# Kernel tuning notes

Measured on AMD Instinct MI355X. Metric: run time of the kernel, lower is better.

The kernel has to match this reference:

```python
import jax, jax.numpy as jnp
import numpy as np


def setup_inputs() -> dict:
    key = jax.random.key(0)
    k1, k2 = jax.random.split(key)
    N, D_IN, D_OUT, R = 500000, 128, 128, 8
    inputs = jax.random.normal(k1, (N, D_IN), dtype=jnp.float32)
    # glorot-uniform-ish init for relation weights
    limit = np.sqrt(6.0 / (D_IN + D_OUT)).astype(np.float32)
    relation_weights = jax.random.uniform(k2, (R, D_IN, D_OUT), dtype=jnp.float32, minval=-limit, maxval=limit)
    relation_scales = jnp.ones((R, 1), dtype=jnp.float32)
    return {"inputs": inputs, "relation_weights": relation_weights, "relation_scales": relation_scales}


def reference(inputs, relation_weights, relation_scales):
    # Original: sum_i  inputs @ (W_i * s_i)
    # Algebraically identical: inputs @ sum_i (W_i * s_i) -> one GEMM.
    # scales: [R,1] -> broadcast over [R, d_in, d_out]
    W_eff = jnp.sum(relation_weights * relation_scales[:, :, None], axis=0)  # [d_in, d_out]
    return inputs @ W_eff  # [N, d_out]
```

## Files before the change

### kernel.cpp

```cpp
#include <hip/hip_runtime.h>

typedef __attribute__((ext_vector_type(8))) short short8;
typedef __attribute__((ext_vector_type(4))) float f32x4;

__device__ __forceinline__ short f2bf(float f) {
    unsigned u = __builtin_bit_cast(unsigned, f);
    u += 0x7fffu + ((u >> 16) & 1u);
    return (short)(u >> 16);
}

__global__ void weff_kernel(const float* __restrict__ W,
                            const float* __restrict__ S,
                            short* __restrict__ WT) {
    int idx = blockIdx.x * 256 + threadIdx.x;
    int k = idx >> 7;
    int n = idx & 127;
    float acc = 0.f;
#pragma unroll
    for (int r = 0; r < 8; ++r) acc += S[r] * W[r * 16384 + idx];
    WT[n * 128 + k] = f2bf(acc);
}

#define BSTRIDE 136

__global__ __launch_bounds__(256, 4) void gemm_kernel(const float* __restrict__ A,
                                                      const short* __restrict__ WT,
                                                      float* __restrict__ C,
                                                      int N) {
    __shared__ __align__(16) short Bs[128 * BSTRIDE];

    int tid = threadIdx.x;
#pragma unroll
    for (int it = 0; it < 8; ++it) {
        int chunk = it * 256 + tid;
        int n  = chunk >> 4;
        int kc = chunk & 15;
        *(short8*)&Bs[n * BSTRIDE + kc * 8] = ((const short8*)WT)[chunk];
    }
    __syncthreads();

    int wave = tid >> 6;
    int lane = tid & 63;
    int quad = lane >> 4;
    int r16  = lane & 15;

    long m0   = (long)blockIdx.x * 64 + wave * 16;
    long rowA = m0 + r16;
    long rowAc = rowA < N ? rowA : (long)(N - 1);
    const float* arow = A + rowAc * 128;

    f32x4 acc[8];
#pragma unroll
    for (int t = 0; t < 8; ++t) acc[t] = (f32x4)(0.f);

#pragma unroll
    for (int kk = 0; kk < 4; ++kk) {
        int k = kk * 32 + quad * 8;
        float4 p = *(const float4*)(arow + k);
        float4 q = *(const float4*)(arow + k + 4);
        short8 afrag;
        afrag[0] = f2bf(p.x); afrag[1] = f2bf(p.y);
        afrag[2] = f2bf(p.z); afrag[3] = f2bf(p.w);
        afrag[4] = f2bf(q.x); afrag[5] = f2bf(q.y);
        afrag[6] = f2bf(q.z); afrag[7] = f2bf(q.w);
#pragma unroll
        for (int t = 0; t < 8; ++t) {
            short8 bfrag = *(const short8*)&Bs[(t * 16 + r16) * BSTRIDE + k];
            acc[t] = __builtin_amdgcn_mfma_f32_16x16x32_bf16(afrag, bfrag, acc[t], 0, 0, 0);
        }
    }

#pragma unroll
    for (int reg = 0; reg < 4; ++reg) {
        long row = m0 + quad * 4 + reg;
        if (row < N) {
            float* crow = C + row * 128;
#pragma unroll
            for (int t = 0; t < 8; ++t) crow[t * 16 + r16] = acc[t][reg];
        }
    }
}

extern "C" void kernel_launch(void* const* d_in, const int* in_sizes, int n_in,
                              void* d_out, int out_size, void* d_ws, size_t ws_size,
                              hipStream_t stream) {
    const float* inputs = (const float*)d_in[0];
    const float* W      = (const float*)d_in[1];
    const float* S      = (const float*)d_in[2];
    float* out = (float*)d_out;
    short* WT  = (short*)d_ws;

    int N = in_sizes[0] / 128;

    weff_kernel<<<64, 256, 0, stream>>>(W, S, WT);
    int grid = (N + 63) / 64;
    gemm_kernel<<<grid, 256, 0, stream>>>(inputs, WT, out, N);
}
```

Baseline: 416.2 us.

## Double rows per wave and stage output through LDS for vectorized stores

Each wave now computes two 16-row M fragments, so every B fragment read from LDS feeds two MFMAs and each block covers 128 rows, which halves the number of blocks and the per-block B staging. The epilogue writes accumulators into padded LDS and then emits coalesced 16-byte global stores per row, replacing scattered 4-byte stores. The cost is more accumulator registers (64 floats per thread), which could reduce occupancy under the launch bounds, plus an extra barrier and an LDS round trip in the epilogue.

```diff
diff --git a/kernel.cpp b/kernel.cpp
--- a/kernel.cpp
+++ b/kernel.cpp
@@ -22,12 +22,15 @@
 }
 
 #define BSTRIDE 136
+#define CSTRIDE 132
+#define SMEM_BYTES 34816
 
 __global__ __launch_bounds__(256, 4) void gemm_kernel(const float* __restrict__ A,
                                                       const short* __restrict__ WT,
                                                       float* __restrict__ C,
                                                       int N) {
-    __shared__ __align__(16) short Bs[128 * BSTRIDE];
+    __shared__ __align__(16) unsigned char smem[SMEM_BYTES];
+    short* Bs = (short*)smem;
 
     int tid = threadIdx.x;
 #pragma unroll
@@ -44,39 +47,63 @@
     int quad = lane >> 4;
     int r16  = lane & 15;
 
-    long m0   = (long)blockIdx.x * 64 + wave * 16;
-    long rowA = m0 + r16;
-    long rowAc = rowA < N ? rowA : (long)(N - 1);
-    const float* arow = A + rowAc * 128;
+    long m0 = (long)blockIdx.x * 128 + wave * 32;
 
-    f32x4 acc[8];
+    const float* arow[2];
 #pragma unroll
-    for (int t = 0; t < 8; ++t) acc[t] = (f32x4)(0.f);
+    for (int mf = 0; mf < 2; ++mf) {
+        long r = m0 + mf * 16 + r16;
+        long rc = r < N ? r : (long)(N - 1);
+        arow[mf] = A + rc * 128;
+    }
+
+    f32x4 acc[2][8];
+#pragma unroll
+    for (int mf = 0; mf < 2; ++mf)
+#pragma unroll
+        for (int t = 0; t < 8; ++t) acc[mf][t] = (f32x4)(0.f);
 
 #pragma unroll
     for (int kk = 0; kk < 4; ++kk) {
         int k = kk * 32 + quad * 8;
-        float4 p = *(const float4*)(arow + k);
-        float4 q = *(const float4*)(arow + k + 4);
-        short8 afrag;
-        afrag[0] = f2bf(p.x); afrag[1] = f2bf(p.y);
-        afrag[2] = f2bf(p.z); afrag[3] = f2bf(p.w);
-        afrag[4] = f2bf(q.x); afrag[5] = f2bf(q.y);
-        afrag[6] = f2bf(q.z); afrag[7] = f2bf(q.w);
+        short8 af[2];
+#pragma unroll
+        for (int mf = 0; mf < 2; ++mf) {
+            float4 p = *(const float4*)(arow[mf] + k);
+            float4 q = *(const float4*)(arow[mf] + k + 4);
+            af[mf][0] = f2bf(p.x); af[mf][1] = f2bf(p.y);
+            af[mf][2] = f2bf(p.z); af[mf][3] = f2bf(p.w);
+            af[mf][4] = f2bf(q.x); af[mf][5] = f2bf(q.y);
+            af[mf][6] = f2bf(q.z); af[mf][7] = f2bf(q.w);
+        }
 #pragma unroll
         for (int t = 0; t < 8; ++t) {
-            short8 bfrag = *(const short8*)&Bs[(t * 16 + r16) * BSTRIDE + k];
-            acc[t] = __builtin_amdgcn_mfma_f32_16x16x32_bf16(afrag, bfrag, acc[t], 0, 0, 0);
+            short8 bf = *(const short8*)&Bs[(t * 16 + r16) * BSTRIDE + k];
+            acc[0][t] = __builtin_amdgcn_mfma_f32_16x16x32_bf16(af[0], bf, acc[0][t], 0, 0, 0);
+            acc[1][t] = __builtin_amdgcn_mfma_f32_16x16x32_bf16(af[1], bf, acc[1][t], 0, 0, 0);
         }
     }
 
+    __syncthreads();
+    float* Cs = (float*)smem + wave * 16 * CSTRIDE;
+
 #pragma unroll
-    for (int reg = 0; reg < 4; ++reg) {
-        long row = m0 + quad * 4 + reg;
-        if (row < N) {
-            float* crow = C + row * 128;
+    for (int mf = 0; mf < 2; ++mf) {
 #pragma unroll
-            for (int t = 0; t < 8; ++t) crow[t * 16 + r16] = acc[t][reg];
+        for (int reg = 0; reg < 4; ++reg)
+#pragma unroll
+            for (int t = 0; t < 8; ++t)
+                Cs[(quad * 4 + reg) * CSTRIDE + t * 16 + r16] = acc[mf][t][reg];
+
+        long gm0 = m0 + mf * 16;
+#pragma unroll
+        for (int j = 0; j < 8; ++j) {
+            int c  = j * 64 + lane;
+            int rl = c >> 5;
+            int c4 = (c & 31) * 4;
+            f32x4 v = *(f32x4*)&Cs[rl * CSTRIDE + c4];
+            long row = gm0 + rl;
+            if (row < N) *(f32x4*)(C + row * 128 + c4) = v;
         }
     }
 }
@@ -93,6 +120,6 @@
     int N = in_sizes[0] / 128;
 
     weff_kernel<<<64, 256, 0, stream>>>(W, S, WT);
-    int grid = (N + 63) / 64;
+    int grid = (N + 127) / 128;
     gemm_kernel<<<grid, 256, 0, stream>>>(inputs, WT, out, N);
 }
```

Measured after the change: 427.4 us. 1.03x slower.
